# Kernel tuning notes

Measured on AMD Instinct MI355X. Metric: run time of the kernel, lower is better.

## Reference

```python
import jax, jax.numpy as jnp
import numpy as np

# Forest of B complete binary trees: L leaves, NPT = 2L-1 nodes per tree.
B, L, H = 128, 512, 128
NPT = 2 * L - 1
N = B * NPT
VOCAB, OUT = 32000, 128


def _levels():
    """Static topo schedule: per internal level, (node, left_child, right_child) global ids."""
    tree_off = np.arange(B, dtype=np.int32)[:, None] * NPT  # [B,1]
    levels = []
    off, cnt = 0, L
    while cnt > 1:
        child_off = off
        off += cnt
        cnt //= 2
        node = off + np.arange(cnt, dtype=np.int32)
        left = child_off + 2 * np.arange(cnt, dtype=np.int32)
        right = left + 1
        levels.append(tuple(jnp.asarray((a[None, :] + tree_off).ravel())
                            for a in (node, left, right)))
    roots = jnp.asarray((tree_off[:, 0] + (NPT - 1)).astype(np.int32))
    leaves = jnp.asarray((np.arange(L, dtype=np.int32)[None, :] + tree_off).ravel())
    return levels, roots, leaves


def setup_inputs() -> dict:
    key = jax.random.key(0)
    ks = jax.random.split(key, 8)
    s = lambda k, shp, sc: jax.random.normal(k, shp, jnp.float32) * sc
    return {
        "label": jax.random.randint(ks[0], (N,), 0, VOCAB),
        "emb": s(ks[1], (VOCAB, H), 0.02),
        "W_iou": s(ks[2], (H, 3 * H), H ** -0.5),
        "U_iou": s(ks[3], (2 * H, 3 * H), (2 * H) ** -0.5),
        "b_iou": jnp.zeros((3 * H,), jnp.float32),
        "U_f_w": s(ks[4], (2 * H, 2 * H), (2 * H) ** -0.5),
        "U_f_b": jnp.zeros((2 * H,), jnp.float32),
        "W_out": s(ks[5], (H, OUT), H ** -0.5),
        "b_out": jnp.zeros((OUT,), jnp.float32),
    }


def _apply_node(iou, b_iou, c_in):
    # apply_node_func: gates + LSTM cell update
    i, o, u = jnp.split(iou + b_iou, 3, axis=-1)
    c = jax.nn.sigmoid(i) * jnp.tanh(u) + c_in
    h = jax.nn.sigmoid(o) * jnp.tanh(c)
    return h, c


def reference(label, emb, W_iou, U_iou, b_iou, U_f_w, U_f_b, W_out, b_out):
    levels, roots, leaves = _levels()
    iou0 = emb[label] @ W_iou                      # [N, 3H] W_iou(emb(label)) for every node
    h = jnp.zeros((N, H), iou0.dtype)
    c = jnp.zeros((N, H), iou0.dtype)
    # leaves: no incoming messages, c_in = 0
    hl, cl = _apply_node(iou0[leaves], b_iou, 0.0)
    h = h.at[leaves].set(hl)
    c = c.at[leaves].set(cl)
    # internal frontiers in topological order (fan-in = 2)
    for node, left, right in levels:
        h_cat = jnp.concatenate([h[left], h[right]], axis=-1)   # [n_d, 2H]
        f = jax.nn.sigmoid(h_cat @ U_f_w + U_f_b)               # forget gates per child
        fl, fr = jnp.split(f, 2, axis=-1)
        c_red = fl * c[left] + fr * c[right]                    # child-sum of gated cells
        iou = h_cat @ U_iou                                     # reduce_func overwrites iou
        hn, cn = _apply_node(iou, b_iou, c_red)
        h = h.at[node].set(hn)
        c = c.at[node].set(cn)
    final = h[roots] @ W_out + b_out                            # root hidden per tree
    return jax.nn.log_softmax(final, axis=-1)
```

## Files before the change

### kernel.cpp

```cpp
#include <hip/hip_runtime.h>
#include <math.h>

#define B_    128
#define L_    512
#define H_    128
#define NPT_  1023
#define N_    (B_ * NPT_)
#define NLEAF (B_ * L_)
#define OUT_  128
#define VOCAB 32000
#define TBASE 960

typedef unsigned short ushort_t;
typedef __attribute__((ext_vector_type(8))) __bf16 bf16x8;
typedef __attribute__((ext_vector_type(4))) float f32x4;

__device__ __forceinline__ float sigmoidf_(float x) {
    return 1.0f / (1.0f + __expf(-x));
}
__device__ __forceinline__ float tanhf_(float x) {
    return 1.0f - 2.0f / (__expf(2.0f * x) + 1.0f);
}
__device__ __forceinline__ ushort_t f2bf(float f) {
    unsigned u = __float_as_uint(f);
    return (ushort_t)((u + 0x7fffu + ((u >> 16) & 1u)) >> 16);
}
__device__ __forceinline__ float bf2f(ushort_t s) {
    return __uint_as_float(((unsigned)s) << 16);
}

__global__ __launch_bounds__(256)
void prep_fused(const float* __restrict__ W_iou,
                const float* __restrict__ U_iou,
                const float* __restrict__ U_f_w,
                const float* __restrict__ emb,
                ushort_t* __restrict__ W_iouT,
                ushort_t* __restrict__ U_catT,
                ushort_t* __restrict__ embb) {
    int idx = blockIdx.x * 256 + threadIdx.x;
    if (idx < VOCAB * H_ / 8) {
        int e0 = idx * 8;
        f32x4 f0 = *(const f32x4*)(emb + e0);
        f32x4 f1 = *(const f32x4*)(emb + e0 + 4);
        union { bf16x8 v; ushort_t e[8]; } p;
        p.e[0] = f2bf(f0[0]); p.e[1] = f2bf(f0[1]);
        p.e[2] = f2bf(f0[2]); p.e[3] = f2bf(f0[3]);
        p.e[4] = f2bf(f1[0]); p.e[5] = f2bf(f1[1]);
        p.e[6] = f2bf(f1[2]); p.e[7] = f2bf(f1[3]);
        *(bf16x8*)(embb + e0) = p.v;
    }
    if (idx < 640 * 256) {
        int n = idx >> 8, k = idx & 255;
        float v = (n < 384) ? U_iou[k * 384 + n] : U_f_w[k * 256 + (n - 384)];
        U_catT[idx] = f2bf(v);
    }
    if (idx < 384 * 128) {
        int n = idx >> 7, k = idx & 127;
        W_iouT[idx] = f2bf(W_iou[k * 384 + n]);
    }
}

__global__ __launch_bounds__(256, 4)
void leaf_v3(const int* __restrict__ label,
             const ushort_t* __restrict__ embb,
             const ushort_t* __restrict__ WT,
             const float* __restrict__ b_iou,
             ushort_t* __restrict__ h,
             float* __restrict__ c) {
    const int tid  = threadIdx.x;
    const int lane = tid & 63;
    const int wave = tid >> 6;
    const int li   = lane & 15;
    const int q    = lane >> 4;
    const int q8   = q << 3;
    const int gg   = blockIdx.y * 4 + wave;
    const int j    = gg * 16 + li;

    bf16x8 Bf[3][4];
    #pragma unroll
    for (int t = 0; t < 3; ++t) {
        const ushort_t* bp = WT + (size_t)(16 * (gg + 8 * t) + li) * 128 + q8;
        #pragma unroll
        for (int kt = 0; kt < 4; ++kt) Bf[t][kt] = *(const bf16x8*)(bp + kt * 32);
    }

    int lab[8];
    #pragma unroll
    for (int t = 0; t < 8; ++t) {
        int ia = (blockIdx.x + t * 512) * 16 + li;
        int ba = ia >> 9, pa = ia & 511;
        lab[t] = label[ba * NPT_ + pa];
    }

    const float bi = b_iou[j], bo = b_iou[128 + j], bu = b_iou[256 + j];

    #pragma unroll 1
    for (int t8 = 0; t8 < 8; ++t8) {
        const int tile = blockIdx.x + t8 * 512;
        const int i0 = tile * 16;
        const ushort_t* pA = embb + (size_t)lab[t8] * H_;
        bf16x8 a[4];
        #pragma unroll
        for (int kt = 0; kt < 4; ++kt) a[kt] = *(const bf16x8*)(pA + kt * 32 + q8);

        f32x4 acc[3];
        #pragma unroll
        for (int t = 0; t < 3; ++t) acc[t] = (f32x4){0.f, 0.f, 0.f, 0.f};
        #pragma unroll
        for (int kt = 0; kt < 4; ++kt)
            #pragma unroll
            for (int t = 0; t < 3; ++t)
                acc[t] = __builtin_amdgcn_mfma_f32_16x16x32_bf16(a[kt], Bf[t][kt], acc[t], 0, 0, 0);

        #pragma unroll
        for (int r = 0; r < 4; ++r) {
            int m  = i0 + q * 4 + r;
            int b  = m >> 9, pos = m & 511;
            size_t gn = (size_t)(b * NPT_ + pos) * H_ + j;
            float iv = sigmoidf_(acc[0][r] + bi);
            float ov = sigmoidf_(acc[1][r] + bo);
            float uv = tanhf_(acc[2][r] + bu);
            float cv = iv * uv;
            float hv = ov * tanhf_(cv);
            c[gn] = cv;
            h[gn] = f2bf(hv);
        }
    }
}

__global__ __launch_bounds__(256, 2)
void level_v32(const ushort_t* __restrict__ Ucat,
               const float* __restrict__ b_iou,
               const float* __restrict__ U_f_b,
               ushort_t* __restrict__ h,
               float* __restrict__ c,
               int node_base, int child_base, int lc,
               int ntiles, int stripes) {
    const int tid  = threadIdx.x;
    const int lane = tid & 63;
    const int wave = tid >> 6;
    const int li   = lane & 15;
    const int q    = lane >> 4;
    const int q8   = q << 3;
    const int mask = (1 << lc) - 1;
    const int gg   = blockIdx.y * 4 + wave;
    const int j    = gg * 16 + li;

    bf16x8 Bf[5][8];
    #pragma unroll
    for (int t = 0; t < 5; ++t) {
        const ushort_t* bp = Ucat + (size_t)(16 * (gg + 8 * t) + li) * 256 + q8;
        #pragma unroll
        for (int kt = 0; kt < 8; ++kt) Bf[t][kt] = *(const bf16x8*)(bp + kt * 32);
    }

    const float bi  = b_iou[j], bo = b_iou[128 + j], bu = b_iou[256 + j];
    const float bfl = U_f_b[j], bfr = U_f_b[128 + j];

    #pragma unroll 1
    for (int tile = blockIdx.x; tile < ntiles; tile += stripes) {
        const int i0 = tile * 32;

        float clv[2][4], crv[2][4];
        int   gnrow[2][4];
        #pragma unroll
        for (int sub = 0; sub < 2; ++sub) {
            #pragma unroll
            for (int r = 0; r < 4; ++r) {
                int m = i0 + sub * 16 + q * 4 + r;
                int b = m >> lc, pos = m & mask;
                int gl = b * NPT_ + child_base + 2 * pos;
                gnrow[sub][r] = b * NPT_ + node_base + pos;
                clv[sub][r] = c[(size_t)gl * H_ + j];
                crv[sub][r] = c[(size_t)(gl + 1) * H_ + j];
            }
        }

        const ushort_t *pl[2], *pr[2];
        #pragma unroll
        for (int sub = 0; sub < 2; ++sub) {
            int ia = i0 + sub * 16 + li, ba = ia >> lc, pa = ia & mask;
            int gl0 = ba * NPT_ + child_base + 2 * pa;
            pl[sub] = h + (size_t)gl0 * H_;
            pr[sub] = h + (size_t)(gl0 + 1) * H_;
        }

        f32x4 acc[2][5];
        #pragma unroll
        for (int s = 0; s < 2; ++s)
            #pragma unroll
            for (int t = 0; t < 5; ++t) acc[s][t] = (f32x4){0.f, 0.f, 0.f, 0.f};

        #pragma unroll
        for (int kt = 0; kt < 8; ++kt) {
            const int ko = (kt & 3) * 32 + q8;
            bf16x8 a0 = *(const bf16x8*)(((kt < 4) ? pl[0] : pr[0]) + ko);
            bf16x8 a1 = *(const bf16x8*)(((kt < 4) ? pl[1] : pr[1]) + ko);
            #pragma unroll
            for (int t = 0; t < 5; ++t) {
                acc[0][t] = __builtin_amdgcn_mfma_f32_16x16x32_bf16(a0, Bf[t][kt], acc[0][t], 0, 0, 0);
                acc[1][t] = __builtin_amdgcn_mfma_f32_16x16x32_bf16(a1, Bf[t][kt], acc[1][t], 0, 0, 0);
            }
        }

        #pragma unroll
        for (int sub = 0; sub < 2; ++sub) {
            #pragma unroll
            for (int r = 0; r < 4; ++r) {
                size_t gn = (size_t)gnrow[sub][r] * H_ + j;
                float iv = sigmoidf_(acc[sub][0][r] + bi);
                float ov = sigmoidf_(acc[sub][1][r] + bo);
                float uv = tanhf_(acc[sub][2][r] + bu);
                float fl = sigmoidf_(acc[sub][3][r] + bfl);
                float fr = sigmoidf_(acc[sub][4][r] + bfr);
                float cv = iv * uv + fl * clv[sub][r] + fr * crv[sub][r];
                float hv = ov * tanhf_(cv);
                c[gn] = cv;
                h[gn] = f2bf(hv);
            }
        }
    }
}

#define TPAD 132
__global__ __launch_bounds__(512, 2)
void tail_kernel(const ushort_t* __restrict__ Ucat,
                 const float* __restrict__ b_iou,
                 const float* __restrict__ U_f_b,
                 const ushort_t* __restrict__ h,
                 const float* __restrict__ c,
                 const float* __restrict__ W_out,
                 const float* __restrict__ b_out,
                 float* __restrict__ out) {
    __shared__ ushort_t hl[63][TPAD];
    __shared__ float    cl[63][TPAD];
    __shared__ float    ev[H_];
    __shared__ float    red[128];

    const int tid  = threadIdx.x;
    const int lane = tid & 63;
    const int wave = tid >> 6;
    const int li   = lane & 15;
    const int q    = lane >> 4;
    const int q8   = q << 3;
    const int gg   = wave;
    const int j    = gg * 16 + li;
    const int b    = blockIdx.x;

    bf16x8 Bf[5][8];
    #pragma unroll
    for (int t = 0; t < 5; ++t) {
        const ushort_t* bp = Ucat + (size_t)(16 * (gg + 8 * t) + li) * 256 + q8;
        #pragma unroll
        for (int kt = 0; kt < 8; ++kt) Bf[t][kt] = *(const bf16x8*)(bp + kt * 32);
    }

    const float bi  = b_iou[j], bo = b_iou[128 + j], bu = b_iou[256 + j];
    const float bfl = U_f_b[j], bfr = U_f_b[128 + j];

    int base = TBASE, child = 896, cnt = 32;
    #pragma unroll 1
    for (int lvl = 0; lvl < 6; ++lvl) {
        const int tiles = (cnt + 15) >> 4;
        for (int tile = 0; tile < tiles; ++tile) {
            const int i0 = tile * 16;

            int pos = i0 + li; if (pos >= cnt) pos = cnt - 1;
            bf16x8 a[8];
            if (lvl == 0) {
                int gl0 = b * NPT_ + child + 2 * pos;
                const ushort_t* pl = h + (size_t)gl0 * H_;
                const ushort_t* pr = h + (size_t)(gl0 + 1) * H_;
                #pragma unroll
                for (int kt = 0; kt < 8; ++kt) {
                    const ushort_t* p = (kt < 4) ? pl : pr;
                    a[kt] = *(const bf16x8*)(p + (kt & 3) * 32 + q8);
                }
            } else {
                int tl = (child - TBASE) + 2 * pos;
                #pragma unroll
                for (int kt = 0; kt < 8; ++kt) {
                    const ushort_t* p = (kt < 4) ? hl[tl] : hl[tl + 1];
                    a[kt] = *(const bf16x8*)(p + (kt & 3) * 32 + q8);
                }
            }

            float clv[4], crv[4];
            #pragma unroll
            for (int r = 0; r < 4; ++r) {
                int m  = i0 + q * 4 + r;
                int pm = m < cnt ? m : cnt - 1;
                if (lvl == 0) {
                    int gl = b * NPT_ + child + 2 * pm;
                    clv[r] = c[(size_t)gl * H_ + j];
                    crv[r] = c[(size_t)(gl + 1) * H_ + j];
                } else {
                    int tl = (child - TBASE) + 2 * pm;
                    clv[r] = cl[tl][j];
                    crv[r] = cl[tl + 1][j];
                }
            }

            f32x4 acc[5];
            #pragma unroll
            for (int t = 0; t < 5; ++t) acc[t] = (f32x4){0.f, 0.f, 0.f, 0.f};
            #pragma unroll
            for (int kt = 0; kt < 8; ++kt)
                #pragma unroll
                for (int t = 0; t < 5; ++t)
                    acc[t] = __builtin_amdgcn_mfma_f32_16x16x32_bf16(a[kt], Bf[t][kt], acc[t], 0, 0, 0);

            #pragma unroll
            for (int r = 0; r < 4; ++r) {
                int m = i0 + q * 4 + r;
                if (m < cnt) {
                    int tl = (base - TBASE) + m;
                    float iv = sigmoidf_(acc[0][r] + bi);
                    float ov = sigmoidf_(acc[1][r] + bo);
                    float uv = tanhf_(acc[2][r] + bu);
                    float fl = sigmoidf_(acc[3][r] + bfl);
                    float fr = sigmoidf_(acc[4][r] + bfr);
                    float cv = iv * uv + fl * clv[r] + fr * crv[r];
                    float hv = ov * tanhf_(cv);
                    cl[tl][j] = cv;
                    hl[tl][j] = f2bf(hv);
                }
            }
        }
        __syncthreads();
        child = base; base += cnt; cnt >>= 1;
    }

    if (tid < 128) ev[tid] = bf2f(hl[62][tid]);
    __syncthreads();

    float acc = 0.0f;
    if (tid < 128) {
        acc = b_out[tid];
        for (int k = 0; k < H_; ++k)
            acc += ev[k] * W_out[k * OUT_ + tid];
        red[tid] = acc;
    }
    __syncthreads();
    for (int s = 64; s > 0; s >>= 1) {
        if (tid < s) red[tid] = fmaxf(red[tid], red[tid + s]);
        __syncthreads();
    }
    float mx = red[0];
    __syncthreads();
    if (tid < 128) red[tid] = expf(acc - mx);
    __syncthreads();
    for (int s = 64; s > 0; s >>= 1) {
        if (tid < s) red[tid] += red[tid + s];
        __syncthreads();
    }
    float lse = logf(red[0]);
    if (tid < 128) out[b * OUT_ + tid] = acc - mx - lse;
}

extern "C" void kernel_launch(void* const* d_in, const int* in_sizes, int n_in,
                              void* d_out, int out_size, void* d_ws, size_t ws_size,
                              hipStream_t stream) {
    const int*   label = (const int*)d_in[0];
    const float* emb   = (const float*)d_in[1];
    const float* W_iou = (const float*)d_in[2];
    const float* U_iou = (const float*)d_in[3];
    const float* b_iou = (const float*)d_in[4];
    const float* U_f_w = (const float*)d_in[5];
    const float* U_f_b = (const float*)d_in[6];
    const float* W_out = (const float*)d_in[7];
    const float* b_out = (const float*)d_in[8];
    float* outp = (float*)d_out;

    float*    c    = (float*)d_ws;
    ushort_t* h    = (ushort_t*)(c + (size_t)N_ * H_);
    ushort_t* Ucat = h + (size_t)N_ * H_;
    ushort_t* WT   = Ucat + 640 * 256;
    ushort_t* embb = WT + 384 * 128;

    prep_fused<<<2000, 256, 0, stream>>>(W_iou, U_iou, U_f_w, emb, WT, Ucat, embb);

    leaf_v3<<<dim3(512, 2), 256, 0, stream>>>(label, embb, WT, b_iou, h, c);

    int child = 0, node = 512, cnt = 256, lc = 8;
    for (int lvl = 0; lvl < 3; ++lvl) {
        int ntiles  = (B_ * cnt) / 32;
        int stripes = ntiles < 256 ? ntiles : 256;
        level_v32<<<dim3(stripes, 2), 256, 0, stream>>>(
            Ucat, b_iou, U_f_b, h, c, node, child, lc, ntiles, stripes);
        child = node; node += cnt; cnt >>= 1; --lc;
    }

    tail_kernel<<<B_, 512, 0, stream>>>(Ucat, b_iou, U_f_b, h, c, W_out, b_out, outp);
}
```

Before: 227.1 us.

## Store cell state in bf16 and stage level weights in shared memory

Cell state c is now stored as bf16 instead of fp32, halving its global memory traffic across the leaf, level and tail kernels. The level kernel stages its 16-column weight slice in padded LDS and has each wave process its own row tiles, instead of holding weights in registers with each wave owning a different column group. The grid changes to 8 column groups by ntiles/8 stripes. This trades LDS reads per MFMA for lower register pressure and less activation re-reading, and reduces cell-state precision.

```diff
diff --git a/kernel.cpp b/kernel.cpp
--- a/kernel.cpp
+++ b/kernel.cpp
@@ -10,6 +10,7 @@
 #define OUT_  128
 #define VOCAB 32000
 #define TBASE 960
+#define BROW  264
 
 typedef unsigned short ushort_t;
 typedef __attribute__((ext_vector_type(8))) __bf16 bf16x8;
@@ -66,7 +67,7 @@
              const ushort_t* __restrict__ WT,
              const float* __restrict__ b_iou,
              ushort_t* __restrict__ h,
-             float* __restrict__ c) {
+             ushort_t* __restrict__ c) {
     const int tid  = threadIdx.x;
     const int lane = tid & 63;
     const int wave = tid >> 6;
@@ -122,20 +123,20 @@
             float uv = tanhf_(acc[2][r] + bu);
             float cv = iv * uv;
             float hv = ov * tanhf_(cv);
-            c[gn] = cv;
+            c[gn] = f2bf(cv);
             h[gn] = f2bf(hv);
         }
     }
 }
 
 __global__ __launch_bounds__(256, 2)
-void level_v32(const ushort_t* __restrict__ Ucat,
+void level_lds(const ushort_t* __restrict__ Ucat,
                const float* __restrict__ b_iou,
                const float* __restrict__ U_f_b,
                ushort_t* __restrict__ h,
-               float* __restrict__ c,
-               int node_base, int child_base, int lc,
-               int ntiles, int stripes) {
+               ushort_t* __restrict__ c,
+               int node_base, int child_base, int lc, int ntiles) {
+    __shared__ ushort_t Bs[5 * 16 * BROW];
     const int tid  = threadIdx.x;
     const int lane = tid & 63;
     const int wave = tid >> 6;
@@ -143,22 +144,27 @@
     const int q    = lane >> 4;
     const int q8   = q << 3;
     const int mask = (1 << lc) - 1;
-    const int gg   = blockIdx.y * 4 + wave;
+    const int gg   = blockIdx.y;
     const int j    = gg * 16 + li;
 
-    bf16x8 Bf[5][8];
     #pragma unroll
-    for (int t = 0; t < 5; ++t) {
-        const ushort_t* bp = Ucat + (size_t)(16 * (gg + 8 * t) + li) * 256 + q8;
-        #pragma unroll
-        for (int kt = 0; kt < 8; ++kt) Bf[t][kt] = *(const bf16x8*)(bp + kt * 32);
-    }
+    for (int it = 0; it < 5; ++it) {
+        int chunk = tid + it * 256;
+        int row = chunk >> 4, seg = chunk & 15;
+        int t = row >> 4, lr = row & 15;
+        const ushort_t* src = Ucat + (size_t)(16 * (gg + 8 * t) + lr) * 256 + seg * 16;
+        ushort_t*       dst = Bs + (t * 16 + lr) * BROW + seg * 16;
+        *(f32x4*)(dst)     = *(const f32x4*)(src);
+        *(f32x4*)(dst + 8) = *(const f32x4*)(src + 8);
+    }
+    __syncthreads();
 
     const float bi  = b_iou[j], bo = b_iou[128 + j], bu = b_iou[256 + j];
     const float bfl = U_f_b[j], bfr = U_f_b[128 + j];
+    const int wstride = gridDim.x * 4;
 
     #pragma unroll 1
-    for (int tile = blockIdx.x; tile < ntiles; tile += stripes) {
+    for (int tile = blockIdx.x * 4 + wave; tile < ntiles; tile += wstride) {
         const int i0 = tile * 32;
 
         float clv[2][4], crv[2][4];
@@ -171,8 +177,8 @@
                 int b = m >> lc, pos = m & mask;
                 int gl = b * NPT_ + child_base + 2 * pos;
                 gnrow[sub][r] = b * NPT_ + node_base + pos;
-                clv[sub][r] = c[(size_t)gl * H_ + j];
-                crv[sub][r] = c[(size_t)(gl + 1) * H_ + j];
+                clv[sub][r] = bf2f(c[(size_t)gl * H_ + j]);
+                crv[sub][r] = bf2f(c[(size_t)(gl + 1) * H_ + j]);
             }
         }
 
@@ -184,22 +190,27 @@
             pl[sub] = h + (size_t)gl0 * H_;
             pr[sub] = h + (size_t)(gl0 + 1) * H_;
         }
-
-        f32x4 acc[2][5];
-        #pragma unroll
-        for (int s = 0; s < 2; ++s)
-            #pragma unroll
-            for (int t = 0; t < 5; ++t) acc[s][t] = (f32x4){0.f, 0.f, 0.f, 0.f};
-
+        bf16x8 a[2][8];
         #pragma unroll
         for (int kt = 0; kt < 8; ++kt) {
             const int ko = (kt & 3) * 32 + q8;
-            bf16x8 a0 = *(const bf16x8*)(((kt < 4) ? pl[0] : pr[0]) + ko);
-            bf16x8 a1 = *(const bf16x8*)(((kt < 4) ? pl[1] : pr[1]) + ko);
+            a[0][kt] = *(const bf16x8*)(((kt < 4) ? pl[0] : pr[0]) + ko);
+            a[1][kt] = *(const bf16x8*)(((kt < 4) ? pl[1] : pr[1]) + ko);
+        }
+
+        f32x4 acc[2][5];
+        #pragma unroll
+        for (int s = 0; s < 2; ++s)
+            #pragma unroll
+            for (int t = 0; t < 5; ++t) acc[s][t] = (f32x4){0.f, 0.f, 0.f, 0.f};
+
+        #pragma unroll
+        for (int kt = 0; kt < 8; ++kt) {
             #pragma unroll
             for (int t = 0; t < 5; ++t) {
-                acc[0][t] = __builtin_amdgcn_mfma_f32_16x16x32_bf16(a0, Bf[t][kt], acc[0][t], 0, 0, 0);
-                acc[1][t] = __builtin_amdgcn_mfma_f32_16x16x32_bf16(a1, Bf[t][kt], acc[1][t], 0, 0, 0);
+                bf16x8 bf = *(const bf16x8*)(Bs + (t * 16 + li) * BROW + kt * 32 + q8);
+                acc[0][t] = __builtin_amdgcn_mfma_f32_16x16x32_bf16(a[0][kt], bf, acc[0][t], 0, 0, 0);
+                acc[1][t] = __builtin_amdgcn_mfma_f32_16x16x32_bf16(a[1][kt], bf, acc[1][t], 0, 0, 0);
             }
         }
 
@@ -215,7 +226,7 @@
                 float fr = sigmoidf_(acc[sub][4][r] + bfr);
                 float cv = iv * uv + fl * clv[sub][r] + fr * crv[sub][r];
                 float hv = ov * tanhf_(cv);
-                c[gn] = cv;
+                c[gn] = f2bf(cv);
                 h[gn] = f2bf(hv);
             }
         }
@@ -228,7 +239,7 @@
                  const float* __restrict__ b_iou,
                  const float* __restrict__ U_f_b,
                  const ushort_t* __restrict__ h,
-                 const float* __restrict__ c,
+                 const ushort_t* __restrict__ c,
                  const float* __restrict__ W_out,
                  const float* __restrict__ b_out,
                  float* __restrict__ out) {
@@ -292,8 +303,8 @@
                 int pm = m < cnt ? m : cnt - 1;
                 if (lvl == 0) {
                     int gl = b * NPT_ + child + 2 * pm;
-                    clv[r] = c[(size_t)gl * H_ + j];
-                    crv[r] = c[(size_t)(gl + 1) * H_ + j];
+                    clv[r] = bf2f(c[(size_t)gl * H_ + j]);
+                    crv[r] = bf2f(c[(size_t)(gl + 1) * H_ + j]);
                 } else {
                     int tl = (child - TBASE) + 2 * pm;
                     clv[r] = cl[tl][j];
@@ -372,8 +383,8 @@
     const float* b_out = (const float*)d_in[8];
     float* outp = (float*)d_out;
 
-    float*    c    = (float*)d_ws;
-    ushort_t* h    = (ushort_t*)(c + (size_t)N_ * H_);
+    ushort_t* c    = (ushort_t*)d_ws;
+    ushort_t* h    = c + (size_t)N_ * H_;
     ushort_t* Ucat = h + (size_t)N_ * H_;
     ushort_t* WT   = Ucat + 640 * 256;
     ushort_t* embb = WT + 384 * 128;
@@ -385,9 +396,9 @@
     int child = 0, node = 512, cnt = 256, lc = 8;
     for (int lvl = 0; lvl < 3; ++lvl) {
         int ntiles  = (B_ * cnt) / 32;
-        int stripes = ntiles < 256 ? ntiles : 256;
-        level_v32<<<dim3(stripes, 2), 256, 0, stream>>>(
-            Ucat, b_iou, U_f_b, h, c, node, child, lc, ntiles, stripes);
+        int stripes = ntiles / 8;
+        level_lds<<<dim3(stripes, 8), 256, 0, stream>>>(
+            Ucat, b_iou, U_f_b, h, c, node, child, lc, ntiles);
         child = node; node += cnt; cnt >>= 1; --lc;
     }
 
```

New measurement: 217.5 us. 1.04x faster.
